# Kernel tuning notes

Hardware: AMD Instinct MI355X
Metric: run time of the kernel (lower is better)

Reference implementation:

```python
import jax, jax.numpy as jnp
import numpy as np

EPS = 1e-5  # BatchNorm2d default eps


def _conv3x3(x, w):
    # x: [B,C,H,W], w: [O,I,3,3], stride 1, 'same' padding (autopad k=3 -> p=1)
    return jax.lax.conv_general_dilated(
        x, w, window_strides=(1, 1), padding=((1, 1), (1, 1)),
        dimension_numbers=("NCHW", "OIHW", "NCHW"))


def _bn(x, g, b, m, v):
    # inference-mode BatchNorm2d with materialized running stats
    scale = (g / jnp.sqrt(v + EPS))[None, :, None, None]
    return (x - m[None, :, None, None]) * scale + b[None, :, None, None]


def _silu(x):
    return x * jax.nn.sigmoid(x)


def _pam(y, q_w, q_b, k_w, k_b, v_w, v_b, pam_gamma):
    # PAM_Module: full pixel-wise self-attention over N = H*W tokens
    B, C, H, W = y.shape
    N = H * W
    yf = y.reshape(B, C, N)
    # 1x1 convs expressed as channel matmuls; q_w: [C//8, C], v_w: [C, C]
    q = jnp.einsum("oc,bcn->bno", q_w, yf) + q_b                 # [B, N, C//8]
    k = jnp.einsum("oc,bcn->bon", k_w, yf) + k_b[None, :, None]  # [B, C//8, N]
    v = jnp.einsum("oc,bcn->bon", v_w, yf) + v_b[None, :, None]  # [B, C, N]
    energy = jnp.einsum("bno,bom->bnm", q, k)                    # [B, N, N]
    attn = jax.nn.softmax(energy, axis=-1)
    # torch: bmm(v, attn.permute(0,2,1)) -> out[b,c,n] = sum_m v[b,c,m] * attn[b,n,m]
    out = jnp.einsum("bcm,bnm->bcn", v, attn).reshape(B, C, H, W)
    return pam_gamma * out + y


def setup_inputs() -> dict:
    key = jax.random.key(0)
    ks = jax.random.split(key, 16)
    B, C1, C2, H, W = 4, 64, 64, 64, 64
    C_ = C2 // 2          # e = 0.5
    C8 = C2 // 8          # PAM q/k channels
    s = 0.05
    inp = {
        "x": jax.random.normal(ks[0], (B, C1, H, W), jnp.float32),
        # cv1: Conv(c1, c_, 3, 1)
        "cv1_w": jax.random.normal(ks[1], (C_, C1, 3, 3), jnp.float32) * s,
        "bn1_g": jax.random.uniform(ks[2], (C_,), jnp.float32, 0.5, 1.5),
        "bn1_b": jax.random.normal(ks[3], (C_,), jnp.float32) * s,
        "bn1_m": jax.random.normal(ks[4], (C_,), jnp.float32) * s,
        "bn1_v": jax.random.uniform(ks[5], (C_,), jnp.float32, 0.5, 1.5),
        # cv2: Conv(c_, c2, 3, 1)
        "cv2_w": jax.random.normal(ks[6], (C2, C_, 3, 3), jnp.float32) * s,
        "bn2_g": jax.random.uniform(ks[7], (C2,), jnp.float32, 0.5, 1.5),
        "bn2_b": jax.random.normal(ks[8], (C2,), jnp.float32) * s,
        "bn2_m": jax.random.normal(ks[9], (C2,), jnp.float32) * s,
        "bn2_v": jax.random.uniform(ks[10], (C2,), jnp.float32, 0.5, 1.5),
        # PAM 1x1 convs (flattened kernels) + biases + gamma
        "q_w": jax.random.normal(ks[11], (C8, C2), jnp.float32) * s,
        "q_b": jax.random.normal(ks[12], (C8,), jnp.float32) * s,
        "k_w": jax.random.normal(ks[13], (C8, C2), jnp.float32) * s,
        "k_b": jax.random.normal(ks[14], (C8,), jnp.float32) * s,
        "v_w": jax.random.normal(ks[15], (C2, C2), jnp.float32) * s,
        "v_b": jnp.zeros((C2,), jnp.float32),
        "pam_gamma": jnp.float32(0.5),  # torch inits 0 (identity); nonzero to exercise path
    }
    return inp


def reference(x, cv1_w, bn1_g, bn1_b, bn1_m, bn1_v,
              cv2_w, bn2_g, bn2_b, bn2_m, bn2_v,
              q_w, q_b, k_w, k_b, v_w, v_b, pam_gamma):
    y = _silu(_bn(_conv3x3(x, cv1_w), bn1_g, bn1_b, bn1_m, bn1_v))   # cv1
    y = _silu(_bn(_conv3x3(y, cv2_w), bn2_g, bn2_b, bn2_m, bn2_v))   # cv2
    # SAA: PAM applied twice on identical input and summed == 2 * PAM(y)
    att = 2.0 * _pam(y, q_w, q_b, k_w, k_b, v_w, v_b, pam_gamma)
    return x + att  # shortcut active (c1 == c2)
```

## Files before the change

kernel.cpp:

```cpp
#include <hip/hip_runtime.h>
#include <hip/hip_bf16.h>

#define NB 4
#define NN 4096

typedef short  bf16x8 __attribute__((ext_vector_type(8)));
typedef float  f32x4  __attribute__((ext_vector_type(4)));

static __device__ __forceinline__ ushort f2bf(float f) {
    unsigned u = __float_as_uint(f);
    u += 0x7fffu + ((u >> 16) & 1u);
    return (ushort)(u >> 16);
}

static __device__ __forceinline__ unsigned cvt_pk_bf16(float a, float b) {
    unsigned r;
    asm("v_cvt_pk_bf16_f32 %0, %1, %2" : "=v"(r) : "v"(a), "v"(b));
    return r;
}

__global__ __launch_bounds__(256) void prep(
    const float* __restrict__ x, const float* __restrict__ w1, const float* __restrict__ w2,
    ushort* __restrict__ xt, ushort* __restrict__ W1r, ushort* __restrict__ W2r)
{
    const int tid = threadIdx.x;
    const int blk = blockIdx.x;
    if (blk < 256) {
        __shared__ float Ts[64][66];
        const int b = blk >> 6, n0 = (blk & 63) * 64;
        const int wv = tid >> 6, lane = tid & 63;
        #pragma unroll
        for (int i = 0; i < 16; ++i) {
            int ci = i * 4 + wv, nn = lane;
            Ts[ci][nn] = x[((size_t)b * 64 + ci) * NN + n0 + nn];
        }
        __syncthreads();
        #pragma unroll
        for (int i = 0; i < 16; ++i) {
            int nn = i * 4 + wv, ci = lane;
            xt[((size_t)b * NN + n0 + nn) * 64 + ci] = f2bf(Ts[ci][nn]);
        }
    } else if (blk < 258) {
        const int base = (blk - 256) * 9216;
        #pragma unroll
        for (int i = 0; i < 36; ++i) {
            int e = base + i * 256 + tid;
            int co = e / 576, k = e % 576, tap = k >> 6, ci = k & 63;
            W1r[e] = f2bf(w1[((size_t)co * 64 + ci) * 9 + tap]);
        }
    } else {
        const int base = (blk - 258) * 9216;
        #pragma unroll
        for (int i = 0; i < 36; ++i) {
            int e = base + i * 256 + tid;
            int co = e / 288, k = e % 288, tap = k >> 5, ci = k & 31;
            W2r[e] = f2bf(w2[((size_t)co * 32 + ci) * 9 + tap]);
        }
    }
}

__global__ __launch_bounds__(256) void conv1_mfma(
    const ushort* __restrict__ xt, const ushort* __restrict__ W1r,
    const float* __restrict__ bng, const float* __restrict__ bnb,
    const float* __restrict__ bnm, const float* __restrict__ bnv,
    ushort* __restrict__ y1t)
{
    __shared__ __align__(16) ushort As[32 * 600];
    __shared__ __align__(16) ushort Xs[24 * 66 * 8];

    const int tid = threadIdx.x;
    const int h = blockIdx.x, b = blockIdx.y;

    #pragma unroll
    for (int i = 0; i < 9; ++i) {
        int cid = i * 256 + tid;
        int row = cid / 72, off = cid % 72;
        *(uint4*)&As[row * 600 + off * 8] = *(const uint4*)(W1r + (size_t)cid * 8);
    }
    #pragma unroll
    for (int r = 0; r < 3; ++r) {
        int gh = h - 1 + r;
        #pragma unroll
        for (int i = 0; i < 2; ++i) {
            int cid = i * 256 + tid;
            int w_ = cid >> 3, cc = cid & 7;
            uint4 v = {0, 0, 0, 0};
            if ((unsigned)gh < 64u)
                v = *(const uint4*)(xt + ((size_t)(b * NN + gh * 64) * 64) + (size_t)cid * 8);
            *(uint4*)&Xs[((r * 8 + cc) * 66 + (w_ + 1)) * 8] = v;
        }
    }
    if (tid < 48) {
        int r = tid >> 4, q = tid & 15, cc = q >> 1, side = (q & 1) * 65;
        uint4 z = {0, 0, 0, 0};
        *(uint4*)&Xs[((r * 8 + cc) * 66 + side) * 8] = z;
    }
    __syncthreads();

    const int lane = tid & 63, wv = tid >> 6;
    const int quad = lane >> 4, l15 = lane & 15;
    const int ch = wv & 1, ph = wv >> 1;

    f32x4 acc[2] = {{0.f,0.f,0.f,0.f},{0.f,0.f,0.f,0.f}};
    #pragma unroll
    for (int kk = 0; kk < 18; ++kk) {
        const int tap = kk >> 1;
        const int dyr = tap / 3, dx = tap % 3;
        bf16x8 af = *(const bf16x8*)&As[(ch * 16 + l15) * 600 + kk * 32 + quad * 8];
        #pragma unroll
        for (int s = 0; s < 2; ++s) {
            int p = ph * 32 + s * 16 + l15;
            bf16x8 bf = *(const bf16x8*)&Xs[((dyr * 8 + (kk & 1) * 4 + quad) * 66 + p + dx) * 8];
            acc[s] = __builtin_amdgcn_mfma_f32_16x16x32_bf16(af, bf, acc[s], 0, 0, 0);
        }
    }

    const int cb = ch * 16 + quad * 4;
    float sc[4], bs[4];
    #pragma unroll
    for (int r = 0; r < 4; ++r) {
        int co = cb + r;
        sc[r] = bng[co] / sqrtf(bnv[co] + 1e-5f);
        bs[r] = bnb[co] - bnm[co] * sc[r];
    }
    #pragma unroll
    for (int s = 0; s < 2; ++s) {
        int p = ph * 32 + s * 16 + l15;
        float r_[4];
        #pragma unroll
        for (int r = 0; r < 4; ++r) {
            float pre = acc[s][r] * sc[r] + bs[r];
            r_[r] = pre / (1.f + __expf(-pre));
        }
        uint2 st;
        st.x = cvt_pk_bf16(r_[0], r_[1]);
        st.y = cvt_pk_bf16(r_[2], r_[3]);
        *(uint2*)&y1t[((size_t)(b * NN + h * 64 + p)) * 32 + cb] = st;
    }
}

__global__ __launch_bounds__(256) void conv2qkv(
    const ushort* __restrict__ y1t, const ushort* __restrict__ W2r,
    const float* __restrict__ bng, const float* __restrict__ bnb,
    const float* __restrict__ bnm, const float* __restrict__ bnv,
    const float* __restrict__ qw, const float* __restrict__ qb,
    const float* __restrict__ kw, const float* __restrict__ kb,
    const float* __restrict__ vw, const float* __restrict__ vb,
    float* __restrict__ y, ushort* __restrict__ q8,
    ushort* __restrict__ ko, ushort* __restrict__ vt)
{
    __shared__ __align__(16) ushort As[64 * 312];
    __shared__ __align__(16) ushort Xs[12 * 66 * 8];
    __shared__ __align__(16) ushort Yt[64 * 76];
    __shared__ __align__(16) ushort Wq[80 * 76];
    __shared__ float Bv[80];

    const int tid = threadIdx.x;
    const int h = blockIdx.x, b = blockIdx.y;

    #pragma unroll
    for (int i = 0; i < 9; ++i) {
        int cid = i * 256 + tid;
        int row = cid / 36, off = cid % 36;
        *(uint4*)&As[row * 312 + off * 8] = *(const uint4*)(W2r + (size_t)cid * 8);
    }
    #pragma unroll
    for (int r = 0; r < 3; ++r) {
        int gh = h - 1 + r;
        int cid = tid;
        int w_ = cid >> 2, cc = cid & 3;
        uint4 v = {0, 0, 0, 0};
        if ((unsigned)gh < 64u)
            v = *(const uint4*)(y1t + ((size_t)(b * NN + gh * 64) * 32) + (size_t)cid * 8);
        *(uint4*)&Xs[((r * 4 + cc) * 66 + (w_ + 1)) * 8] = v;
    }
    if (tid < 24) {
        int r = tid >> 3, q = tid & 7, cc = q >> 1, side = (q & 1) * 65;
        uint4 z = {0, 0, 0, 0};
        *(uint4*)&Xs[((r * 4 + cc) * 66 + side) * 8] = z;
    }
    for (int i = tid; i < 2560; i += 256) {
        int chw = i >> 5, c2 = (i & 31) * 2;
        const float* src = (chw < 8) ? (qw + chw * 64 + c2)
                         : (chw < 16) ? (kw + (chw - 8) * 64 + c2)
                         : (vw + (chw - 16) * 64 + c2);
        float2 v2 = *(const float2*)src;
        *(unsigned*)&Wq[chw * 76 + c2] = cvt_pk_bf16(v2.x, v2.y);
    }
    if (tid < 80) Bv[tid] = (tid < 8) ? qb[tid] : (tid < 16) ? kb[tid - 8] : vb[tid - 16];
    __syncthreads();

    const int lane = tid & 63, wv = tid >> 6;
    const int quad = lane >> 4, l15 = lane & 15;

    f32x4 acc[4] = {{0.f,0.f,0.f,0.f},{0.f,0.f,0.f,0.f},{0.f,0.f,0.f,0.f},{0.f,0.f,0.f,0.f}};
    #pragma unroll
    for (int kk = 0; kk < 9; ++kk) {
        const int dyr = kk / 3, dx = kk % 3;
        bf16x8 af = *(const bf16x8*)&As[(wv * 16 + l15) * 312 + kk * 32 + quad * 8];
        #pragma unroll
        for (int s = 0; s < 4; ++s) {
            int p = s * 16 + l15;
            bf16x8 bf = *(const bf16x8*)&Xs[((dyr * 4 + quad) * 66 + p + dx) * 8];
            acc[s] = __builtin_amdgcn_mfma_f32_16x16x32_bf16(af, bf, acc[s], 0, 0, 0);
        }
    }

    const int cb = wv * 16 + quad * 4;
    float sc[4], bs[4];
    #pragma unroll
    for (int r = 0; r < 4; ++r) {
        int co = cb + r;
        sc[r] = bng[co] / sqrtf(bnv[co] + 1e-5f);
        bs[r] = bnb[co] - bnm[co] * sc[r];
    }
    #pragma unroll
    for (int s = 0; s < 4; ++s) {
        int p = s * 16 + l15;
        #pragma unroll
        for (int r = 0; r < 4; ++r) {
            float pre = acc[s][r] * sc[r] + bs[r];
            float res = pre / (1.f + __expf(-pre));
            y[((size_t)(b * 64 + cb + r)) * NN + h * 64 + p] = res;
            Yt[p * 76 + cb + r] = f2bf(res);
        }
    }
    __syncthreads();

    bf16x8 aY0 = *(const bf16x8*)&Yt[(wv * 16 + l15) * 76 + quad * 8];
    bf16x8 aY1 = *(const bf16x8*)&Yt[(wv * 16 + l15) * 76 + 32 + quad * 8];
    const int nbase = h * 64 + wv * 16 + quad * 4;
    const int vtile = h * 2 + (wv >> 1);
    const int vslot = quad * 8 + (wv & 1) * 4;
    #pragma unroll
    for (int cht = 0; cht < 5; ++cht) {
        bf16x8 bW0 = *(const bf16x8*)&Wq[(cht * 16 + l15) * 76 + quad * 8];
        bf16x8 bW1 = *(const bf16x8*)&Wq[(cht * 16 + l15) * 76 + 32 + quad * 8];
        f32x4 qa = {0.f, 0.f, 0.f, 0.f};
        qa = __builtin_amdgcn_mfma_f32_16x16x32_bf16(aY0, bW0, qa, 0, 0, 0);
        qa = __builtin_amdgcn_mfma_f32_16x16x32_bf16(aY1, bW1, qa, 0, 0, 0);
        const float bias = Bv[cht * 16 + l15];
        const int chn = cht * 16 + l15;
        if (cht == 0) {
            if (l15 < 8) {
                #pragma unroll
                for (int r = 0; r < 4; ++r)
                    q8[((size_t)b * NN + nbase + r) * 8 + chn] = f2bf(qa[r] + bias);
            } else {
                #pragma unroll
                for (int r = 0; r < 4; ++r)
                    ko[((size_t)b * NN + nbase + r) * 8 + (chn - 8)] = f2bf(qa[r] + bias);
            }
        } else {
            const int c = chn - 16;
            uint2 st;
            st.x = cvt_pk_bf16(qa[0] + bias, qa[1] + bias);
            st.y = cvt_pk_bf16(qa[2] + bias, qa[3] + bias);
            *(uint2*)&vt[(((size_t)(b * 128 + vtile)) * 64 + c) * 32 + vslot] = st;
        }
    }
}

__global__ __launch_bounds__(512, 2) void flash_pam(
    const ushort* __restrict__ q8,
    const ushort* __restrict__ k8,
    const ushort* __restrict__ vt,
    const float* __restrict__ y,
    const float* __restrict__ x,
    const float* __restrict__ gamma_p,
    float* __restrict__ out)
{
    __shared__ __align__(16) float Osum[4 * 4352];
    __shared__ float Lw[8][64];
    __shared__ float Ls[64];

    const int tid = threadIdx.x;
    const int bx = blockIdx.x;
    const int b  = bx >> 6;
    const int nt = bx & 63;
    const int n0 = nt * 64;

    const int lane = tid & 63, w = tid >> 6;
    const int quad = lane >> 4, l15 = lane & 15;

    const uint4 z4 = {0u, 0u, 0u, 0u};

    bf16x8 bQ[4];
    #pragma unroll
    for (int af = 0; af < 4; ++af) {
        uint4 qv = *(const uint4*)(q8 + ((size_t)b * NN + n0 + af * 16 + l15) * 8);
        uint4 sel = (quad == 0) ? qv : z4;
        bQ[af] = *(bf16x8*)&sel;
    }

    const ushort* kg = k8 + ((size_t)b * NN + w * 512) * 8;
    const ushort* vg = vt + ((size_t)(b * 128 + w * 16)) * 64 * 32;

    f32x4 acc[4][4];
    #pragma unroll
    for (int af = 0; af < 4; ++af)
        #pragma unroll
        for (int ct = 0; ct < 4; ++ct)
            acc[af][ct] = (f32x4){0.f, 0.f, 0.f, 0.f};
    float lacc[4] = {0.f, 0.f, 0.f, 0.f};
    const f32x4 zf = {0.f, 0.f, 0.f, 0.f};

    #pragma unroll 2
    for (int t = 0; t < 16; ++t) {
        const int g = t * 32;
        bf16x8 aK0 = *(const bf16x8*)(kg + (size_t)(g + l15) * 8);
        bf16x8 aK1 = *(const bf16x8*)(kg + (size_t)(g + 16 + l15) * 8);

        bf16x8 vb_[4];
        #pragma unroll
        for (int ct = 0; ct < 4; ++ct)
            vb_[ct] = *(const bf16x8*)(vg + (size_t)t * 2048 + (ct * 16 + l15) * 32 + quad * 8);

        #pragma unroll
        for (int af = 0; af < 4; ++af) {
            f32x4 s0 = __builtin_amdgcn_mfma_f32_16x16x32_bf16(aK0, bQ[af], zf, 0, 0, 0);
            f32x4 s1 = __builtin_amdgcn_mfma_f32_16x16x32_bf16(aK1, bQ[af], zf, 0, 0, 0);

            float e[8];
            #pragma unroll
            for (int r = 0; r < 4; ++r) {
                e[r]     = __expf(s0[r]);
                e[4 + r] = __expf(s1[r]);
            }
            #pragma unroll
            for (int r = 0; r < 8; ++r) lacc[af] += e[r];
            union { unsigned u[4]; bf16x8 v; } pk;
            pk.u[0] = cvt_pk_bf16(e[0], e[1]);
            pk.u[1] = cvt_pk_bf16(e[2], e[3]);
            pk.u[2] = cvt_pk_bf16(e[4], e[5]);
            pk.u[3] = cvt_pk_bf16(e[6], e[7]);

            #pragma unroll
            for (int ct = 0; ct < 4; ++ct)
                acc[af][ct] = __builtin_amdgcn_mfma_f32_16x16x32_bf16(pk.v, vb_[ct], acc[af][ct], 0, 0, 0);
        }
    }

    #pragma unroll
    for (int af = 0; af < 4; ++af) {
        lacc[af] += __shfl_xor(lacc[af], 16, 64);
        lacc[af] += __shfl_xor(lacc[af], 32, 64);
    }
    if (quad == 0) {
        #pragma unroll
        for (int af = 0; af < 4; ++af)
            Lw[w][af * 16 + l15] = lacc[af];
    }

    if (w >= 4) {
        #pragma unroll
        for (int af = 0; af < 4; ++af)
            #pragma unroll
            for (int ct = 0; ct < 4; ++ct)
                *(f32x4*)&Osum[(w - 4) * 4352 + (ct * 16 + l15) * 68 + af * 16 + quad * 4] = acc[af][ct];
    }
    __syncthreads();
    if (w < 4) {
        #pragma unroll
        for (int af = 0; af < 4; ++af)
            #pragma unroll
            for (int ct = 0; ct < 4; ++ct) {
                float* p = &Osum[w * 4352 + (ct * 16 + l15) * 68 + af * 16 + quad * 4];
                f32x4 v = *(const f32x4*)p;
                *(f32x4*)p = v + acc[af][ct];
            }
    }
    if (tid < 64) {
        float s = Lw[0][tid] + Lw[1][tid] + Lw[2][tid] + Lw[3][tid]
                + Lw[4][tid] + Lw[5][tid] + Lw[6][tid] + Lw[7][tid];
        Ls[tid] = 1.0f / s;
    }
    __syncthreads();

    {
        const int c = tid >> 3, n8 = (tid & 7) * 8;
        f32x4 o0 = {0.f, 0.f, 0.f, 0.f}, o1 = {0.f, 0.f, 0.f, 0.f};
        #pragma unroll
        for (int s = 0; s < 4; ++s) {
            o0 += *(const f32x4*)&Osum[s * 4352 + c * 68 + n8];
            o1 += *(const f32x4*)&Osum[s * 4352 + c * 68 + n8 + 4];
        }
        const float g2 = 2.f * gamma_p[0];
        const size_t idx = ((size_t)b * 64 + c) * NN + n0 + n8;
        f32x4 xv0 = *(const f32x4*)(x + idx);
        f32x4 xv1 = *(const f32x4*)(x + idx + 4);
        f32x4 yv0 = *(const f32x4*)(y + idx);
        f32x4 yv1 = *(const f32x4*)(y + idx + 4);
        f32x4 r0, r1;
        #pragma unroll
        for (int u = 0; u < 4; ++u) {
            r0[u] = xv0[u] + 2.f * yv0[u] + g2 * o0[u] * Ls[n8 + u];
            r1[u] = xv1[u] + 2.f * yv1[u] + g2 * o1[u] * Ls[n8 + 4 + u];
        }
        *(f32x4*)(out + idx) = r0;
        *(f32x4*)(out + idx + 4) = r1;
    }
}

extern "C" void kernel_launch(void* const* d_in, const int* in_sizes, int n_in,
                              void* d_out, int out_size, void* d_ws, size_t ws_size,
                              hipStream_t stream) {
    const float* x    = (const float*)d_in[0];
    const float* w1   = (const float*)d_in[1];
    const float* g1   = (const float*)d_in[2];
    const float* b1   = (const float*)d_in[3];
    const float* m1   = (const float*)d_in[4];
    const float* v1   = (const float*)d_in[5];
    const float* w2   = (const float*)d_in[6];
    const float* g2   = (const float*)d_in[7];
    const float* b2   = (const float*)d_in[8];
    const float* m2   = (const float*)d_in[9];
    const float* v2   = (const float*)d_in[10];
    const float* qw   = (const float*)d_in[11];
    const float* qb   = (const float*)d_in[12];
    const float* kw   = (const float*)d_in[13];
    const float* kb   = (const float*)d_in[14];
    const float* vw   = (const float*)d_in[15];
    const float* vb   = (const float*)d_in[16];
    const float* gam  = (const float*)d_in[17];
    float* outp = (float*)d_out;

    float* ws = (float*)d_ws;
    ushort* xt  = (ushort*)ws;
    float*  y   = ws + 524288;
    ushort* q8  = (ushort*)(ws + 1572864);
    ushort* kk  = (ushort*)(ws + 1703936);
    ushort* vv  = (ushort*)(ws + 1769472);
    float*  S   = ws + 2326528;
    ushort* y1t = (ushort*)S;
    ushort* W1r = (ushort*)(S + 262144);
    ushort* W2r = (ushort*)(S + 271360);

    prep<<<260, 256, 0, stream>>>(x, w1, w2, xt, W1r, W2r);
    conv1_mfma<<<dim3(64, NB), 256, 0, stream>>>(xt, W1r, g1, b1, m1, v1, y1t);
    conv2qkv<<<dim3(64, NB), 256, 0, stream>>>(y1t, W2r, g2, b2, m2, v2,
                                               qw, qb, kw, kb, vw, vb,
                                               y, q8, kk, vv);
    flash_pam<<<256, 512, 0, stream>>>(q8, kk, vv, y, x, gam, outp);
}
```

Measured before the change: 128.2 us.

## Fuse input/weight prep into conv kernels and double threads per block

Removes the separate prep kernel by having conv1 read fp32 NCHW input and fp32 weights directly, converting to bf16 while staging into shared memory, and conv2 likewise converts its weights in place. Both conv kernels move from 256 to 512 threads, splitting the MFMA output tiles and the QKV projection across twice as many waves. This saves one launch and an intermediate round trip through global memory. In exchange every block redundantly reconverts the weights with strided fp32 loads.

```diff
diff --git a/kernel.cpp b/kernel.cpp
--- a/kernel.cpp
+++ b/kernel.cpp
@@ -19,48 +19,8 @@
     return r;
 }
 
-__global__ __launch_bounds__(256) void prep(
-    const float* __restrict__ x, const float* __restrict__ w1, const float* __restrict__ w2,
-    ushort* __restrict__ xt, ushort* __restrict__ W1r, ushort* __restrict__ W2r)
-{
-    const int tid = threadIdx.x;
-    const int blk = blockIdx.x;
-    if (blk < 256) {
-        __shared__ float Ts[64][66];
-        const int b = blk >> 6, n0 = (blk & 63) * 64;
-        const int wv = tid >> 6, lane = tid & 63;
-        #pragma unroll
-        for (int i = 0; i < 16; ++i) {
-            int ci = i * 4 + wv, nn = lane;
-            Ts[ci][nn] = x[((size_t)b * 64 + ci) * NN + n0 + nn];
-        }
-        __syncthreads();
-        #pragma unroll
-        for (int i = 0; i < 16; ++i) {
-            int nn = i * 4 + wv, ci = lane;
-            xt[((size_t)b * NN + n0 + nn) * 64 + ci] = f2bf(Ts[ci][nn]);
-        }
-    } else if (blk < 258) {
-        const int base = (blk - 256) * 9216;
-        #pragma unroll
-        for (int i = 0; i < 36; ++i) {
-            int e = base + i * 256 + tid;
-            int co = e / 576, k = e % 576, tap = k >> 6, ci = k & 63;
-            W1r[e] = f2bf(w1[((size_t)co * 64 + ci) * 9 + tap]);
-        }
-    } else {
-        const int base = (blk - 258) * 9216;
-        #pragma unroll
-        for (int i = 0; i < 36; ++i) {
-            int e = base + i * 256 + tid;
-            int co = e / 288, k = e % 288, tap = k >> 5, ci = k & 31;
-            W2r[e] = f2bf(w2[((size_t)co * 32 + ci) * 9 + tap]);
-        }
-    }
-}
-
-__global__ __launch_bounds__(256) void conv1_mfma(
-    const ushort* __restrict__ xt, const ushort* __restrict__ W1r,
+__global__ __launch_bounds__(512) void conv1_mfma(
+    const float* __restrict__ x, const float* __restrict__ w1,
     const float* __restrict__ bng, const float* __restrict__ bnb,
     const float* __restrict__ bnm, const float* __restrict__ bnv,
     ushort* __restrict__ y1t)
@@ -71,23 +31,38 @@
     const int tid = threadIdx.x;
     const int h = blockIdx.x, b = blockIdx.y;
 
-    #pragma unroll
-    for (int i = 0; i < 9; ++i) {
-        int cid = i * 256 + tid;
-        int row = cid / 72, off = cid % 72;
-        *(uint4*)&As[row * 600 + off * 8] = *(const uint4*)(W1r + (size_t)cid * 8);
-    }
-    #pragma unroll
-    for (int r = 0; r < 3; ++r) {
-        int gh = h - 1 + r;
-        #pragma unroll
-        for (int i = 0; i < 2; ++i) {
-            int cid = i * 256 + tid;
-            int w_ = cid >> 3, cc = cid & 7;
-            uint4 v = {0, 0, 0, 0};
-            if ((unsigned)gh < 64u)
-                v = *(const uint4*)(xt + ((size_t)(b * NN + gh * 64) * 64) + (size_t)cid * 8);
-            *(uint4*)&Xs[((r * 8 + cc) * 66 + (w_ + 1)) * 8] = v;
+    for (int cid = tid; cid < 2304; cid += 512) {
+        const int row = cid / 72, off = cid % 72;
+        const int k0 = off * 8;
+        const int tap = k0 >> 6, ci0 = k0 & 63;
+        float v[8];
+        #pragma unroll
+        for (int j = 0; j < 8; ++j)
+            v[j] = w1[((size_t)(row * 64 + ci0 + j)) * 9 + tap];
+        union { unsigned u[4]; uint4 q; } pk;
+        #pragma unroll
+        for (int j = 0; j < 4; ++j) pk.u[j] = cvt_pk_bf16(v[2*j], v[2*j+1]);
+        *(uint4*)&As[row * 600 + off * 8] = pk.q;
+    }
+
+    {
+        const int nn = tid & 63, cc = tid >> 6;
+        #pragma unroll
+        for (int r = 0; r < 3; ++r) {
+            const int gh = h - 1 + r;
+            float v[8];
+            if ((unsigned)gh < 64u) {
+                #pragma unroll
+                for (int sub = 0; sub < 8; ++sub)
+                    v[sub] = x[(((size_t)b * 64 + cc * 8 + sub) * 64 + gh) * 64 + nn];
+            } else {
+                #pragma unroll
+                for (int sub = 0; sub < 8; ++sub) v[sub] = 0.f;
+            }
+            union { unsigned u[4]; uint4 q; } pk;
+            #pragma unroll
+            for (int j = 0; j < 4; ++j) pk.u[j] = cvt_pk_bf16(v[2*j], v[2*j+1]);
+            *(uint4*)&Xs[((r * 8 + cc) * 66 + (nn + 1)) * 8] = pk.q;
         }
     }
     if (tid < 48) {
@@ -99,48 +74,38 @@
 
     const int lane = tid & 63, wv = tid >> 6;
     const int quad = lane >> 4, l15 = lane & 15;
-    const int ch = wv & 1, ph = wv >> 1;
-
-    f32x4 acc[2] = {{0.f,0.f,0.f,0.f},{0.f,0.f,0.f,0.f}};
+    const int ch = wv & 1, ph2 = wv >> 1;
+
+    const int p = ph2 * 16 + l15;
+
+    f32x4 acc = {0.f, 0.f, 0.f, 0.f};
     #pragma unroll
     for (int kk = 0; kk < 18; ++kk) {
         const int tap = kk >> 1;
         const int dyr = tap / 3, dx = tap % 3;
         bf16x8 af = *(const bf16x8*)&As[(ch * 16 + l15) * 600 + kk * 32 + quad * 8];
-        #pragma unroll
-        for (int s = 0; s < 2; ++s) {
-            int p = ph * 32 + s * 16 + l15;
-            bf16x8 bf = *(const bf16x8*)&Xs[((dyr * 8 + (kk & 1) * 4 + quad) * 66 + p + dx) * 8];
-            acc[s] = __builtin_amdgcn_mfma_f32_16x16x32_bf16(af, bf, acc[s], 0, 0, 0);
-        }
+        bf16x8 bf = *(const bf16x8*)&Xs[((dyr * 8 + (kk & 1) * 4 + quad) * 66 + p + dx) * 8];
+        acc = __builtin_amdgcn_mfma_f32_16x16x32_bf16(af, bf, acc, 0, 0, 0);
     }
 
     const int cb = ch * 16 + quad * 4;
-    float sc[4], bs[4];
+    float r_[4];
     #pragma unroll
     for (int r = 0; r < 4; ++r) {
         int co = cb + r;
-        sc[r] = bng[co] / sqrtf(bnv[co] + 1e-5f);
-        bs[r] = bnb[co] - bnm[co] * sc[r];
-    }
-    #pragma unroll
-    for (int s = 0; s < 2; ++s) {
-        int p = ph * 32 + s * 16 + l15;
-        float r_[4];
-        #pragma unroll
-        for (int r = 0; r < 4; ++r) {
-            float pre = acc[s][r] * sc[r] + bs[r];
-            r_[r] = pre / (1.f + __expf(-pre));
-        }
-        uint2 st;
-        st.x = cvt_pk_bf16(r_[0], r_[1]);
-        st.y = cvt_pk_bf16(r_[2], r_[3]);
-        *(uint2*)&y1t[((size_t)(b * NN + h * 64 + p)) * 32 + cb] = st;
-    }
-}
-
-__global__ __launch_bounds__(256) void conv2qkv(
-    const ushort* __restrict__ y1t, const ushort* __restrict__ W2r,
+        float sc = bng[co] / sqrtf(bnv[co] + 1e-5f);
+        float bs = bnb[co] - bnm[co] * sc;
+        float pre = acc[r] * sc + bs;
+        r_[r] = pre / (1.f + __expf(-pre));
+    }
+    uint2 st;
+    st.x = cvt_pk_bf16(r_[0], r_[1]);
+    st.y = cvt_pk_bf16(r_[2], r_[3]);
+    *(uint2*)&y1t[((size_t)(b * NN + h * 64 + p)) * 32 + cb] = st;
+}
+
+__global__ __launch_bounds__(512) void conv2qkv(
+    const ushort* __restrict__ y1t, const float* __restrict__ w2,
     const float* __restrict__ bng, const float* __restrict__ bnb,
     const float* __restrict__ bnm, const float* __restrict__ bnv,
     const float* __restrict__ qw, const float* __restrict__ qb,
@@ -158,17 +123,24 @@
     const int tid = threadIdx.x;
     const int h = blockIdx.x, b = blockIdx.y;
 
-    #pragma unroll
-    for (int i = 0; i < 9; ++i) {
-        int cid = i * 256 + tid;
-        int row = cid / 36, off = cid % 36;
-        *(uint4*)&As[row * 312 + off * 8] = *(const uint4*)(W2r + (size_t)cid * 8);
-    }
-    #pragma unroll
-    for (int r = 0; r < 3; ++r) {
-        int gh = h - 1 + r;
-        int cid = tid;
-        int w_ = cid >> 2, cc = cid & 3;
+    for (int cid = tid; cid < 2304; cid += 512) {
+        const int row = cid / 36, off = cid % 36;
+        const int k0 = off * 8;
+        const int tap = k0 >> 5, ci0 = k0 & 31;
+        float v[8];
+        #pragma unroll
+        for (int j = 0; j < 8; ++j)
+            v[j] = w2[((size_t)(row * 32 + ci0 + j)) * 9 + tap];
+        union { unsigned u[4]; uint4 q; } pk;
+        #pragma unroll
+        for (int j = 0; j < 4; ++j) pk.u[j] = cvt_pk_bf16(v[2*j], v[2*j+1]);
+        *(uint4*)&As[row * 312 + off * 8] = pk.q;
+    }
+
+    for (int it = tid; it < 768; it += 512) {
+        const int r = it >> 8, cid = it & 255;
+        const int gh = h - 1 + r;
+        const int w_ = cid >> 2, cc = cid & 3;
         uint4 v = {0, 0, 0, 0};
         if ((unsigned)gh < 64u)
             v = *(const uint4*)(y1t + ((size_t)(b * NN + gh * 64) * 32) + (size_t)cid * 8);
@@ -179,7 +151,7 @@
         uint4 z = {0, 0, 0, 0};
         *(uint4*)&Xs[((r * 4 + cc) * 66 + side) * 8] = z;
     }
-    for (int i = tid; i < 2560; i += 256) {
+    for (int i = tid; i < 2560; i += 512) {
         int chw = i >> 5, c2 = (i & 31) * 2;
         const float* src = (chw < 8) ? (qw + chw * 64 + c2)
                          : (chw < 16) ? (kw + (chw - 8) * 64 + c2)
@@ -192,21 +164,22 @@
 
     const int lane = tid & 63, wv = tid >> 6;
     const int quad = lane >> 4, l15 = lane & 15;
-
-    f32x4 acc[4] = {{0.f,0.f,0.f,0.f},{0.f,0.f,0.f,0.f},{0.f,0.f,0.f,0.f},{0.f,0.f,0.f,0.f}};
+    const int ct2 = wv & 3, phh = wv >> 2;
+
+    f32x4 acc[2] = {{0.f,0.f,0.f,0.f},{0.f,0.f,0.f,0.f}};
     #pragma unroll
     for (int kk = 0; kk < 9; ++kk) {
         const int dyr = kk / 3, dx = kk % 3;
-        bf16x8 af = *(const bf16x8*)&As[(wv * 16 + l15) * 312 + kk * 32 + quad * 8];
-        #pragma unroll
-        for (int s = 0; s < 4; ++s) {
-            int p = s * 16 + l15;
+        bf16x8 af = *(const bf16x8*)&As[(ct2 * 16 + l15) * 312 + kk * 32 + quad * 8];
+        #pragma unroll
+        for (int s = 0; s < 2; ++s) {
+            int p = phh * 32 + s * 16 + l15;
             bf16x8 bf = *(const bf16x8*)&Xs[((dyr * 4 + quad) * 66 + p + dx) * 8];
             acc[s] = __builtin_amdgcn_mfma_f32_16x16x32_bf16(af, bf, acc[s], 0, 0, 0);
         }
     }
 
-    const int cb = wv * 16 + quad * 4;
+    const int cb = ct2 * 16 + quad * 4;
     float sc[4], bs[4];
     #pragma unroll
     for (int r = 0; r < 4; ++r) {
@@ -215,8 +188,8 @@
         bs[r] = bnb[co] - bnm[co] * sc[r];
     }
     #pragma unroll
-    for (int s = 0; s < 4; ++s) {
-        int p = s * 16 + l15;
+    for (int s = 0; s < 2; ++s) {
+        int p = phh * 32 + s * 16 + l15;
         #pragma unroll
         for (int r = 0; r < 4; ++r) {
             float pre = acc[s][r] * sc[r] + bs[r];
@@ -227,13 +200,15 @@
     }
     __syncthreads();
 
-    bf16x8 aY0 = *(const bf16x8*)&Yt[(wv * 16 + l15) * 76 + quad * 8];
-    bf16x8 aY1 = *(const bf16x8*)&Yt[(wv * 16 + l15) * 76 + 32 + quad * 8];
-    const int nbase = h * 64 + wv * 16 + quad * 4;
-    const int vtile = h * 2 + (wv >> 1);
-    const int vslot = quad * 8 + (wv & 1) * 4;
-    #pragma unroll
-    for (int cht = 0; cht < 5; ++cht) {
+    const int pg = wv & 3;
+    bf16x8 aY0 = *(const bf16x8*)&Yt[(pg * 16 + l15) * 76 + quad * 8];
+    bf16x8 aY1 = *(const bf16x8*)&Yt[(pg * 16 + l15) * 76 + 32 + quad * 8];
+    const int nbase = h * 64 + pg * 16 + quad * 4;
+    const int vtile = h * 2 + (pg >> 1);
+    const int vslot = quad * 8 + (pg & 1) * 4;
+    const int cht0 = (wv < 4) ? 0 : 3;
+    const int chtN = (wv < 4) ? 3 : 5;
+    for (int cht = cht0; cht < chtN; ++cht) {
         bf16x8 bW0 = *(const bf16x8*)&Wq[(cht * 16 + l15) * 76 + quad * 8];
         bf16x8 bW1 = *(const bf16x8*)&Wq[(cht * 16 + l15) * 76 + 32 + quad * 8];
         f32x4 qa = {0.f, 0.f, 0.f, 0.f};
@@ -426,19 +401,15 @@
     float* outp = (float*)d_out;
 
     float* ws = (float*)d_ws;
-    ushort* xt  = (ushort*)ws;
     float*  y   = ws + 524288;
     ushort* q8  = (ushort*)(ws + 1572864);
     ushort* kk  = (ushort*)(ws + 1703936);
     ushort* vv  = (ushort*)(ws + 1769472);
     float*  S   = ws + 2326528;
     ushort* y1t = (ushort*)S;
-    ushort* W1r = (ushort*)(S + 262144);
-    ushort* W2r = (ushort*)(S + 271360);
-
-    prep<<<260, 256, 0, stream>>>(x, w1, w2, xt, W1r, W2r);
-    conv1_mfma<<<dim3(64, NB), 256, 0, stream>>>(xt, W1r, g1, b1, m1, v1, y1t);
-    conv2qkv<<<dim3(64, NB), 256, 0, stream>>>(y1t, W2r, g2, b2, m2, v2,
+
+    conv1_mfma<<<dim3(64, NB), 512, 0, stream>>>(x, w1, g1, b1, m1, v1, y1t);
+    conv2qkv<<<dim3(64, NB), 512, 0, stream>>>(y1t, w2, g2, b2, m2, v2,
                                                qw, qb, kw, kb, vw, vb,
                                                y, q8, kk, vv);
     flash_pam<<<256, 512, 0, stream>>>(q8, kk, vv, y, x, gam, outp);
```

Measured after the change: 129.2 us. Within noise of the previous version (+0.8%).
